# Optimization experiments

Measured on AMD Instinct MI355X. Metric: run time of the kernel, lower is better.

Reference implementation:

```python
import jax, jax.numpy as jnp
import numpy as np

N = 100000        # nodes
E = 1_600_000     # edges (avg degree 16)
F_IN = 128        # in_channels
HID = 64          # hidden_channels (per-head)
H1 = 4            # heads layer 1
G = 128           # number of graphs
NEG_SLOPE = 0.2   # PyG GATConv default leaky_relu slope


def setup_inputs() -> dict:
    key = jax.random.key(0)
    ks = jax.random.split(key, 12)
    x = jax.random.normal(ks[0], (N, F_IN), dtype=jnp.float32)
    edge_index = jax.random.randint(ks[1], (2, E), 0, N, dtype=jnp.int64)
    batch = jnp.sort(jax.random.randint(ks[2], (N,), 0, G, dtype=jnp.int64))
    s1 = 1.0 / np.sqrt(F_IN)
    s2 = 1.0 / np.sqrt(H1 * HID)
    # layer 1: in=F_IN, out=H1*HID (PyG lin has no bias; separate bias after concat)
    w1 = jax.random.normal(ks[3], (H1 * HID, F_IN), dtype=jnp.float32) * s1
    a_src1 = jax.random.normal(ks[4], (H1, HID), dtype=jnp.float32) * s1
    a_dst1 = jax.random.normal(ks[5], (H1, HID), dtype=jnp.float32) * s1
    b1 = jnp.zeros((H1 * HID,), dtype=jnp.float32)
    # layer 2: in=H1*HID, out=HID, heads=1
    w2 = jax.random.normal(ks[6], (1 * HID, H1 * HID), dtype=jnp.float32) * s2
    a_src2 = jax.random.normal(ks[7], (1, HID), dtype=jnp.float32) * s2
    a_dst2 = jax.random.normal(ks[8], (1, HID), dtype=jnp.float32) * s2
    b2 = jnp.zeros((HID,), dtype=jnp.float32)
    return {"x": x, "w1": w1, "a_src1": a_src1, "a_dst1": a_dst1, "b1": b1,
            "w2": w2, "a_src2": a_src2, "a_dst2": a_dst2, "b2": b2,
            "edge_index": edge_index, "batch": batch}


def _segment_softmax(alpha, seg, n):
    # numerically-stable softmax of alpha [E,H] grouped by seg (dst node)
    m = jax.ops.segment_max(alpha, seg, num_segments=n)
    m = jnp.where(jnp.isfinite(m), m, 0.0)  # empty segments -> 0
    a = jnp.exp(alpha - m[seg])
    s = jax.ops.segment_sum(a, seg, num_segments=n)
    return a / (s[seg] + 1e-16)


def _gat_conv(x, w, a_src, a_dst, bias, src, dst, n, heads, ch):
    h = (x @ w.T).reshape(n, heads, ch)          # [N,H,C]
    alpha_src = jnp.sum(h * a_src[None], axis=-1)  # [N,H]
    alpha_dst = jnp.sum(h * a_dst[None], axis=-1)  # [N,H]
    e = jax.nn.leaky_relu(alpha_src[src] + alpha_dst[dst], NEG_SLOPE)  # [E,H]
    att = _segment_softmax(e, dst, n)             # [E,H]
    msg = h[src] * att[:, :, None]                # [E,H,C]
    out = jax.ops.segment_sum(msg, dst, num_segments=n)  # [N,H,C]
    return out.reshape(n, heads * ch) + bias


def reference(x, w1, a_src1, a_dst1, b1, w2, a_src2, a_dst2, b2, edge_index, batch):
    src, dst = edge_index[0], edge_index[1]
    h = jax.nn.relu(_gat_conv(x, w1, a_src1, a_dst1, b1, src, dst, N, H1, HID))
    h = jax.nn.relu(_gat_conv(h, w2, a_src2, a_dst2, b2, src, dst, N, 1, HID))
    # global_mean_pool over graph ids
    sums = jax.ops.segment_sum(h, batch, num_segments=G)            # [G,HID]
    cnt = jax.ops.segment_sum(jnp.ones((N,), h.dtype), batch, num_segments=G)
    return sums / jnp.maximum(cnt, 1.0)[:, None]
```

## Files before the change

kernel.cpp:

```cpp
#include <hip/hip_runtime.h>
#include <math.h>
#include <type_traits>

#define NNODES 100000
#define NEDGES 1600000
#define NGRAPH 128
#define NBKT 391
#define CAP 1536
#define EPB 2048

typedef _Float16 f16x4 __attribute__((ext_vector_type(4)));
typedef _Float16 f16x8 __attribute__((ext_vector_type(8)));
typedef float f32x4 __attribute__((ext_vector_type(4)));

__global__ __launch_bounds__(256) void front1(
    const float* __restrict__ w1, const float* __restrict__ w2,
    const float* __restrict__ as1c, const float* __restrict__ ad1c,
    const float* __restrict__ as2c, const float* __restrict__ ad2c,
    _Float16* __restrict__ w1h, _Float16* __restrict__ w2h,
    _Float16* __restrict__ va1, _Float16* __restrict__ va2,
    const int* __restrict__ srcv, const int* __restrict__ dstv,
    unsigned* __restrict__ part, int* __restrict__ gcur, int e_count) {
  __shared__ int hist[NBKT];
  __shared__ int base_[NBKT];
  __shared__ int lofs[NBKT];
  const int tid = threadIdx.x;
  if (blockIdx.x < 202) {
    const int b = blockIdx.x;
    if (b < 8) {
      if (tid < 128) {
        int h = b & 3;
        const float* coef = (b >= 4) ? ad1c : as1c;
        float s = 0.f;
        for (int c = 0; c < 64; ++c)
          s = fmaf(w1[(size_t)(h * 64 + c) * 128 + tid], coef[h * 64 + c], s);
        va1[b * 128 + tid] = (_Float16)s;
        va1[(b + 8) * 128 + tid] = (_Float16)0.f;
      }
    } else if (b < 10) {
      int r = b - 8;
      const float* coef = r ? ad2c : as2c;
      float s = 0.f;
      for (int c = 0; c < 64; ++c) s = fmaf(w2[(size_t)c * 256 + tid], coef[c], s);
      va2[r * 256 + tid] = (_Float16)s;
      for (int z = 2 + r * 7; z < 9 + r * 7; ++z) va2[z * 256 + tid] = (_Float16)0.f;
    } else if (b < 138) {
      int i = (b - 10) * 256 + tid;
      w1h[i] = (_Float16)w1[i];
    } else {
      int i = (b - 138) * 256 + tid;
      w2h[i] = (_Float16)w2[i];
    }
    return;
  }
  const int ab = blockIdx.x - 202;
  const int P = ab & 7;
  for (int i = tid; i < NBKT; i += 256) { hist[i] = 0; lofs[i] = 0; }
  __syncthreads();
  const int e0 = ab * EPB;
  const int e1 = min(e0 + EPB, e_count);
  for (int e = e0 + tid; e < e1; e += 256) atomicAdd(&hist[dstv[e] >> 8], 1);
  __syncthreads();
  for (int i = tid; i < NBKT; i += 256) {
    int c = hist[i];
    base_[i] = c ? atomicAdd(&gcur[(P * NBKT + i) * 16], c) : 0;
  }
  __syncthreads();
  for (int e = e0 + tid; e < e1; e += 256) {
    int d = dstv[e];
    int b = d >> 8;
    int l = atomicAdd(&lofs[b], 1);
    part[(size_t)(P * NBKT + b) * CAP + base_[b] + l] =
        ((unsigned)srcv[e] << 8) | (unsigned)(d & 255);
  }
}

__global__ __launch_bounds__(256) void bucketB1p(const unsigned* __restrict__ part,
    const int* __restrict__ gcur, int* __restrict__ pre, int* __restrict__ bsum, int n) {
  __shared__ int cnt[256];
  __shared__ int sc[256];
  const int b = blockIdx.x, tid = threadIdx.x;
  cnt[tid] = 0;
  __syncthreads();
  for (int P = 0; P < 8; ++P) {
    int cn = gcur[(P * NBKT + b) * 16];
    const unsigned* seg = part + (size_t)(P * NBKT + b) * CAP;
    for (int i = tid; i < cn; i += 256) atomicAdd(&cnt[seg[i] & 255], 1);
  }
  __syncthreads();
  int own = cnt[tid];
  sc[tid] = own;
  __syncthreads();
  for (int o = 1; o < 256; o <<= 1) {
    int t = (tid >= o) ? sc[tid - o] : 0;
    __syncthreads();
    sc[tid] += t;
    __syncthreads();
  }
  int node = (b << 8) + tid;
  if (node < n) pre[node] = sc[tid] - own;
  if (tid == 255) bsum[b] = sc[255];
}

__global__ __launch_bounds__(256) void scan23(const int* __restrict__ pre,
    const int* __restrict__ bsum, int* __restrict__ offsets, int n, int e_count) {
  __shared__ int bs[NBKT];
  __shared__ int red[256];
  const int b = blockIdx.x, tid = threadIdx.x;
  for (int i = tid; i < NBKT; i += 256) bs[i] = bsum[i];
  __syncthreads();
  int part_ = 0;
  for (int i = tid; i < b; i += 256) part_ += bs[i];
  red[tid] = part_;
  __syncthreads();
  for (int o = 128; o; o >>= 1) {
    if (tid < o) red[tid] += red[tid + o];
    __syncthreads();
  }
  int base = red[0];
  int node = (b << 8) + tid;
  if (node < n) offsets[node] = base + pre[node];
  if (b == NBKT - 1 && tid == 0) offsets[n] = e_count;
}

__global__ __launch_bounds__(256) void bucketB2(const unsigned* __restrict__ part,
    const int* __restrict__ gcur, const int* __restrict__ offsets,
    int* __restrict__ esrc, int n) {
  __shared__ int lcur[256];
  const int b = blockIdx.x, tid = threadIdx.x;
  int node = (b << 8) + tid;
  lcur[tid] = (node < n) ? offsets[node] : 0;
  __syncthreads();
  for (int P = 0; P < 8; ++P) {
    int cn = gcur[(P * NBKT + b) * 16];
    const unsigned* seg = part + (size_t)(P * NBKT + b) * CAP;
    for (int i = tid; i < cn; i += 256) {
      unsigned e = seg[i];
      int slot = atomicAdd(&lcur[e & 255], 1);
      esrc[slot] = (int)(e >> 8);
    }
  }
}

template <int K, int N, typename AT>
__global__ __launch_bounds__(256) void gemm_mfma(const AT* __restrict__ A,
    const _Float16* __restrict__ Bh, const _Float16* __restrict__ VA,
    _Float16* __restrict__ C, int M, float* __restrict__ asrc, float* __restrict__ adst) {
  constexpr int H = N / 64;
  constexpr int KS = K / 32, NT = N / 16;
  constexpr int BM = 400, NG = 7;
  constexpr int CP = N + 8;
  __shared__ _Float16 Bs[N * K];
  __shared__ _Float16 VAs[16 * K];
  __shared__ _Float16 Cs[64 * CP];
  const int tid = threadIdx.x;
  const int lane = tid & 63, wid = tid >> 6;
  const int lr = lane & 15, lk = (lane >> 4) * 8;
  const int bm = blockIdx.x * BM;

  for (int i = tid * 8; i < N * K; i += 2048) {
    int row = i / K, k = i & (K - 1);
    f16x8 v = *(const f16x8*)&Bh[i];
    *(f16x8*)&Bs[(row * K + k) ^ ((row & 7) << 3)] = v;
  }
  for (int i = tid * 8; i < 16 * K; i += 2048) {
    int row = i / K, k = i & (K - 1);
    f16x8 v = *(const f16x8*)&VA[i];
    *(f16x8*)&VAs[(row * K + k) ^ ((row & 7) << 3)] = v;
  }
  __syncthreads();

  auto loadA = [&](int g, f16x8* areg) {
    int rlocal = g * 64 + wid * 16 + lr;
    int row = bm + rlocal;
    if (rlocal < BM && row < M) {
      const AT* arow = A + (size_t)row * K;
#pragma unroll
      for (int ks = 0; ks < KS; ++ks) {
        if constexpr (std::is_same<AT, float>::value) {
          float4 v0 = *(const float4*)&arow[ks * 32 + lk];
          float4 v1 = *(const float4*)&arow[ks * 32 + lk + 4];
          f16x8 t;
          t[0] = (_Float16)v0.x; t[1] = (_Float16)v0.y; t[2] = (_Float16)v0.z; t[3] = (_Float16)v0.w;
          t[4] = (_Float16)v1.x; t[5] = (_Float16)v1.y; t[6] = (_Float16)v1.z; t[7] = (_Float16)v1.w;
          areg[ks] = t;
        } else {
          areg[ks] = *(const f16x8*)&arow[ks * 32 + lk];
        }
      }
    } else {
#pragma unroll
      for (int ks = 0; ks < KS; ++ks) areg[ks] = (f16x8){};
    }
  };

  f16x8 a[KS], an[KS];
  loadA(0, a);
  const int rl0 = wid * 16 + (lane >> 4) * 4;

  for (int g = 0; g < NG; ++g) {
    if (g + 1 < NG) loadA(g + 1, an);

    f32x4 accv = (f32x4){0.f, 0.f, 0.f, 0.f};
#pragma unroll
    for (int ks = 0; ks < KS; ++ks) {
      f16x8 bv = *(const f16x8*)&VAs[(lr * K + ks * 32 + lk) ^ ((lr & 7) << 3)];
      accv = __builtin_amdgcn_mfma_f32_16x16x32_f16(a[ks], bv, accv, 0, 0, 0);
    }

    f32x4 acc[NT];
#pragma unroll
    for (int nt = 0; nt < NT; ++nt) acc[nt] = (f32x4){0.f, 0.f, 0.f, 0.f};
#pragma unroll
    for (int nt = 0; nt < NT; ++nt) {
      int brow = nt * 16 + lr;
#pragma unroll
      for (int ks = 0; ks < KS; ++ks) {
        f16x8 b = *(const f16x8*)&Bs[(brow * K + ks * 32 + lk) ^ ((brow & 7) << 3)];
        acc[nt] = __builtin_amdgcn_mfma_f32_16x16x32_f16(a[ks], b, acc[nt], 0, 0, 0);
      }
    }

#pragma unroll
    for (int r = 0; r < 4; ++r) {
      int rl = rl0 + r;
#pragma unroll
      for (int nt = 0; nt < NT; ++nt) Cs[rl * CP + nt * 16 + lr] = (_Float16)acc[nt][r];
      int rlocal = g * 64 + rl;
      int row = bm + rlocal;
      if (rlocal < BM && row < M) {
        if (lr < H) asrc[row * H + lr] = accv[r];
        else if (lr < 2 * H) adst[row * H + lr - H] = accv[r];
      }
    }
    __syncthreads();

    int rmax = min(64, min(BM - g * 64, M - (bm + g * 64)));
    if (rmax > 0) {
      int nch = rmax * (N / 8);
      for (int q = tid; q < nch; q += 256) {
        int row = q / (N / 8), c8 = q % (N / 8);
        f16x8 v = *(const f16x8*)&Cs[row * CP + c8 * 8];
        *(f16x8*)&C[(size_t)(bm + g * 64 + row) * N + c8 * 8] = v;
      }
    }
    __syncthreads();
#pragma unroll
    for (int ks = 0; ks < KS; ++ks) a[ks] = an[ks];
  }
}

__global__ __launch_bounds__(256) void agg1_kernel(const _Float16* __restrict__ hmat,
    const float* __restrict__ asrc, const float* __restrict__ adst,
    const int* __restrict__ offsets, const int* __restrict__ esrc,
    const float* __restrict__ bias, _Float16* __restrict__ outv) {
  const int lane = threadIdx.x & 63, wid = threadIdx.x >> 6;
  const int node = blockIdx.x * 4 + wid;
  if (node >= NNODES) return;
  const int h = lane >> 4;
  const int start = offsets[node];
  const int end = offsets[node + 1];
  const float adn = adst[node * 4 + h];
  const _Float16* hbase = hmat + lane * 4;
  float acc[4] = {0.f, 0.f, 0.f, 0.f};
  float s = 0.f;
  int j = start;
  for (; j + 8 <= end; j += 8) {
    int sv[8];
#pragma unroll
    for (int t = 0; t < 8; ++t) sv[t] = esrc[j + t];
    f16x4 vv[8];
#pragma unroll
    for (int t = 0; t < 8; ++t) vv[t] = *(const f16x4*)&hbase[(size_t)sv[t] * 256];
    _Float16 ph[8];
#pragma unroll
    for (int t = 0; t < 8; ++t) {
      float v = asrc[sv[t] * 4 + h] + adn;
      v = (v > 0.f) ? v : 0.2f * v;
      float p = __expf(v);
      s += p;
      ph[t] = (_Float16)p;
    }
#pragma unroll
    for (int t = 0; t < 8; ++t)
#pragma unroll
      for (int k = 0; k < 4; ++k)
        acc[k] = fmaf((float)vv[t][k], (float)ph[t], acc[k]);
  }
  for (; j < end; ++j) {
    int sv = esrc[j];
    f16x4 vv = *(const f16x4*)&hbase[(size_t)sv * 256];
    float v = asrc[sv * 4 + h] + adn;
    v = (v > 0.f) ? v : 0.2f * v;
    float p = __expf(v);
    s += p;
    _Float16 phs = (_Float16)p;
#pragma unroll
    for (int k = 0; k < 4; ++k) acc[k] = fmaf((float)vv[k], (float)phs, acc[k]);
  }
  float inv = 1.f / (s + 1e-16f);
  f16x4 ho;
#pragma unroll
  for (int k = 0; k < 4; ++k)
    ho[k] = (_Float16)fmaxf(fmaf(acc[k], inv, bias[lane * 4 + k]), 0.f);
  *(f16x4*)&outv[(size_t)node * 256 + lane * 4] = ho;
}

__global__ __launch_bounds__(256) void agg2_kernel(const _Float16* __restrict__ hmat,
    const float* __restrict__ asrc, const float* __restrict__ adst,
    const int* __restrict__ offsets, const int* __restrict__ esrc,
    const float* __restrict__ bias, _Float16* __restrict__ outv) {
  const int lane = threadIdx.x & 63, wid = threadIdx.x >> 6;
  const int g = lane >> 4, q = lane & 15;
  const int node = blockIdx.x * 16 + wid * 4 + g;
  if (node >= NNODES) return;
  const int start = offsets[node];
  const int end = offsets[node + 1];
  const float adn = adst[node];
  const _Float16* hbase = hmat + q * 4;
  float acc[4] = {0.f, 0.f, 0.f, 0.f};
  float s = 0.f;
  int j = start;
  for (; j + 8 <= end; j += 8) {
    int sv[8];
#pragma unroll
    for (int t = 0; t < 8; ++t) sv[t] = esrc[j + t];
    f16x4 v[8];
#pragma unroll
    for (int t = 0; t < 8; ++t) v[t] = *(const f16x4*)&hbase[(size_t)sv[t] * 64];
#pragma unroll
    for (int t = 0; t < 8; ++t) {
      float x = asrc[sv[t]] + adn;
      x = (x > 0.f) ? x : 0.2f * x;
      float p = __expf(x);
      s += p;
      _Float16 phs = (_Float16)p;
#pragma unroll
      for (int k = 0; k < 4; ++k) acc[k] = fmaf((float)v[t][k], (float)phs, acc[k]);
    }
  }
  for (; j < end; ++j) {
    int sv = esrc[j];
    f16x4 v = *(const f16x4*)&hbase[(size_t)sv * 64];
    float x = asrc[sv] + adn;
    x = (x > 0.f) ? x : 0.2f * x;
    float p = __expf(x);
    s += p;
    _Float16 phs = (_Float16)p;
#pragma unroll
    for (int k = 0; k < 4; ++k) acc[k] = fmaf((float)v[k], (float)phs, acc[k]);
  }
  float inv = 1.f / (s + 1e-16f);
  f16x4 ho;
#pragma unroll
  for (int k = 0; k < 4; ++k)
    ho[k] = (_Float16)fmaxf(fmaf(acc[k], inv, bias[q * 4 + k]), 0.f);
  *(f16x4*)&outv[(size_t)node * 64 + q * 4] = ho;
}

__global__ __launch_bounds__(256) void pool_kernel(const _Float16* __restrict__ g2,
    const int* __restrict__ batch, float* __restrict__ out, int n) {
  const int gid = blockIdx.x;
  const int lane = threadIdx.x & 63, w = threadIdx.x >> 6;
  int lo = 0, hi = n;
  while (lo < hi) { int mid = (lo + hi) >> 1; if (batch[mid] < gid) lo = mid + 1; else hi = mid; }
  int lb = lo;
  hi = n;
  while (lo < hi) { int mid = (lo + hi) >> 1; if (batch[mid] < gid + 1) lo = mid + 1; else hi = mid; }
  int ub = lo;
  float acc = 0.f;
  for (int i = lb + w; i < ub; i += 4) acc += (float)g2[(size_t)i * 64 + lane];
  __shared__ float red[4][64];
  red[w][lane] = acc;
  __syncthreads();
  if (threadIdx.x < 64) {
    float sum = (red[0][lane] + red[1][lane]) + (red[2][lane] + red[3][lane]);
    float cnt = fmaxf((float)(ub - lb), 1.f);
    out[gid * 64 + lane] = sum / cnt;
  }
}

extern "C" void kernel_launch(void* const* d_in, const int* in_sizes, int n_in,
                              void* d_out, int out_size, void* d_ws, size_t ws_size,
                              hipStream_t stream) {
  const float* x      = (const float*)d_in[0];
  const float* w1     = (const float*)d_in[1];
  const float* a_src1 = (const float*)d_in[2];
  const float* a_dst1 = (const float*)d_in[3];
  const float* b1     = (const float*)d_in[4];
  const float* w2     = (const float*)d_in[5];
  const float* a_src2 = (const float*)d_in[6];
  const float* a_dst2 = (const float*)d_in[7];
  const float* b2     = (const float*)d_in[8];
  const int*   src    = (const int*)d_in[9];
  const int*   dst    = src + NEDGES;
  const int*   batch  = (const int*)d_in[10];
  float* out = (float*)d_out;

  const int N = NNODES, E = NEDGES;

  char* wsb = (char*)d_ws;
  size_t off = 0;
  auto alloc = [&](size_t bytes) {
    void* p = wsb + off;
    off = (off + bytes + 255) & ~(size_t)255;
    return p;
  };
  _Float16* h1h = (_Float16*)alloc((size_t)N * 256 * 2);
  _Float16* g1h = (_Float16*)alloc((size_t)N * 256 * 2);
  _Float16* h2h = (_Float16*)alloc((size_t)N * 64 * 2);
  _Float16* g2h = (_Float16*)alloc((size_t)N * 64 * 2);
  float* as1    = (float*)alloc((size_t)N * 4 * 4);
  float* ad1    = (float*)alloc((size_t)N * 4 * 4);
  float* as2    = (float*)alloc((size_t)N * 4);
  float* ad2    = (float*)alloc((size_t)N * 4);
  int* pre      = (int*)alloc((size_t)N * 4);
  int* bsum     = (int*)alloc((size_t)NBKT * 4);
  int* offsets  = (int*)alloc((size_t)(N + 1) * 4);
  int* esrc     = (int*)alloc((size_t)E * 4);
  unsigned* part= (unsigned*)alloc((size_t)8 * NBKT * CAP * 4);
  int* gcur     = (int*)alloc((size_t)8 * NBKT * 16 * 4);
  _Float16* w1h = (_Float16*)alloc((size_t)256 * 128 * 2);
  _Float16* w2h = (_Float16*)alloc((size_t)64 * 256 * 2);
  _Float16* va1 = (_Float16*)alloc((size_t)16 * 128 * 2);
  _Float16* va2 = (_Float16*)alloc((size_t)16 * 256 * 2);

  hipMemsetAsync(gcur, 0, (size_t)8 * NBKT * 16 * 4, stream);
  front1<<<202 + (E + EPB - 1) / EPB, 256, 0, stream>>>(
      w1, w2, a_src1, a_dst1, a_src2, a_dst2, w1h, w2h, va1, va2,
      src, dst, part, gcur, E);

  bucketB1p<<<NBKT, 256, 0, stream>>>(part, gcur, pre, bsum, N);
  scan23<<<NBKT, 256, 0, stream>>>(pre, bsum, offsets, N, E);
  bucketB2<<<NBKT, 256, 0, stream>>>(part, gcur, offsets, esrc, N);

  gemm_mfma<128, 256, float><<<250, 256, 0, stream>>>(
      x, w1h, va1, h1h, N, as1, ad1);
  agg1_kernel<<<(N + 3) / 4, 256, 0, stream>>>(h1h, as1, ad1, offsets, esrc, b1, g1h);

  gemm_mfma<256, 64, _Float16><<<250, 256, 0, stream>>>(
      g1h, w2h, va2, h2h, N, as2, ad2);
  agg2_kernel<<<(N + 15) / 16, 256, 0, stream>>>(h2h, as2, ad2, offsets, esrc, b2, g2h);

  pool_kernel<<<NGRAPH, 256, 0, stream>>>(g2h, batch, out, N);
}
```

Baseline: 346.2 us.

## Fuse offset scan into bucket scatter, split agg1 launch, add occupancy hints

Result: no change. 352.4 us (+1.8%).

```diff
diff --git a/kernel.cpp b/kernel.cpp
--- a/kernel.cpp
+++ b/kernel.cpp
@@ -102,10 +102,13 @@
   if (tid == 255) bsum[b] = sc[255];
 }
 
-__global__ __launch_bounds__(256) void scan23(const int* __restrict__ pre,
-    const int* __restrict__ bsum, int* __restrict__ offsets, int n, int e_count) {
+__global__ __launch_bounds__(256) void bucketB2(const unsigned* __restrict__ part,
+    const int* __restrict__ gcur, const int* __restrict__ pre,
+    const int* __restrict__ bsum, int* __restrict__ offsets,
+    int* __restrict__ esrc, int n, int e_count) {
   __shared__ int bs[NBKT];
   __shared__ int red[256];
+  __shared__ int lcur[256];
   const int b = blockIdx.x, tid = threadIdx.x;
   for (int i = tid; i < NBKT; i += 256) bs[i] = bsum[i];
   __syncthreads();
@@ -119,17 +122,13 @@
   }
   int base = red[0];
   int node = (b << 8) + tid;
-  if (node < n) offsets[node] = base + pre[node];
+  int ofs = base;
+  if (node < n) {
+    ofs = base + pre[node];
+    offsets[node] = ofs;
+  }
+  lcur[tid] = ofs;
   if (b == NBKT - 1 && tid == 0) offsets[n] = e_count;
-}
-
-__global__ __launch_bounds__(256) void bucketB2(const unsigned* __restrict__ part,
-    const int* __restrict__ gcur, const int* __restrict__ offsets,
-    int* __restrict__ esrc, int n) {
-  __shared__ int lcur[256];
-  const int b = blockIdx.x, tid = threadIdx.x;
-  int node = (b << 8) + tid;
-  lcur[tid] = (node < n) ? offsets[node] : 0;
   __syncthreads();
   for (int P = 0; P < 8; ++P) {
     int cn = gcur[(P * NBKT + b) * 16];
@@ -250,12 +249,12 @@
   }
 }
 
-__global__ __launch_bounds__(256) void agg1_kernel(const _Float16* __restrict__ hmat,
+__global__ __launch_bounds__(256, 8) void agg1_kernel(const _Float16* __restrict__ hmat,
     const float* __restrict__ asrc, const float* __restrict__ adst,
     const int* __restrict__ offsets, const int* __restrict__ esrc,
-    const float* __restrict__ bias, _Float16* __restrict__ outv) {
+    const float* __restrict__ bias, _Float16* __restrict__ outv, int node0) {
   const int lane = threadIdx.x & 63, wid = threadIdx.x >> 6;
-  const int node = blockIdx.x * 4 + wid;
+  const int node = node0 + blockIdx.x * 4 + wid;
   if (node >= NNODES) return;
   const int h = lane >> 4;
   const int start = offsets[node];
@@ -306,7 +305,7 @@
   *(f16x4*)&outv[(size_t)node * 256 + lane * 4] = ho;
 }
 
-__global__ __launch_bounds__(256) void agg2_kernel(const _Float16* __restrict__ hmat,
+__global__ __launch_bounds__(256, 8) void agg2_kernel(const _Float16* __restrict__ hmat,
     const float* __restrict__ asrc, const float* __restrict__ adst,
     const int* __restrict__ offsets, const int* __restrict__ esrc,
     const float* __restrict__ bias, _Float16* __restrict__ outv) {
@@ -431,12 +430,12 @@
       src, dst, part, gcur, E);
 
   bucketB1p<<<NBKT, 256, 0, stream>>>(part, gcur, pre, bsum, N);
-  scan23<<<NBKT, 256, 0, stream>>>(pre, bsum, offsets, N, E);
-  bucketB2<<<NBKT, 256, 0, stream>>>(part, gcur, offsets, esrc, N);
+  bucketB2<<<NBKT, 256, 0, stream>>>(part, gcur, pre, bsum, offsets, esrc, N, E);
 
   gemm_mfma<128, 256, float><<<250, 256, 0, stream>>>(
       x, w1h, va1, h1h, N, as1, ad1);
-  agg1_kernel<<<(N + 3) / 4, 256, 0, stream>>>(h1h, as1, ad1, offsets, esrc, b1, g1h);
+  agg1_kernel<<<12500, 256, 0, stream>>>(h1h, as1, ad1, offsets, esrc, b1, g1h, 0);
+  agg1_kernel<<<12500, 256, 0, stream>>>(h1h, as1, ad1, offsets, esrc, b1, g1h, 50000);
 
   gemm_mfma<256, 64, _Float16><<<250, 256, 0, stream>>>(
       g1h, w2h, va2, h2h, N, as2, ad2);
```
